# Optimization experiments

Hardware: AMD Instinct MI355X
Metric: run time of the kernel (lower is better)

The kernel has to match this reference:

```python
import jax, jax.numpy as jnp
import numpy as np

N = 100000        # total points across all graphs in the batch
NUM_THETAS = 64
BUMP_STEPS = 64
NUM_GRAPHS = 128  # data.batch.max() + 1
R = 1.0


def setup_inputs() -> dict:
    key = jax.random.key(0)
    k1, k2 = jax.random.split(key)
    x = jax.random.normal(k1, (N, 2), dtype=jnp.float32)
    # direction vectors on the circle, as in the module's Parameter init
    t = jnp.linspace(0.0, 2.0 * jnp.pi, NUM_THETAS)
    v = jnp.stack([jnp.sin(t), jnp.cos(t)], axis=1).astype(jnp.float32)  # [T, 2]
    lin = jnp.linspace(-R, R, BUMP_STEPS).astype(jnp.float32)            # [S]
    batch = jnp.sort(jax.random.randint(k2, (N,), 0, NUM_GRAPHS)).astype(jnp.int64)
    return {"x": x, "v": v, "lin": lin, "batch": batch}


def reference(x, v, lin, batch):
    # nh: projection of each point onto each direction -> [N, T]
    nh = x @ v.T
    # sigmoid bump over filtration heights: [S, N, T]
    ecc = jax.nn.sigmoid(200.0 * (lin[:, None, None] - nh[None, :, :]))
    # index_add over point dim keyed by graph id, then movedim(0,1):
    # transpose to [N, S, T] and segment-sum over N -> [B, S, T]
    out = jax.ops.segment_sum(jnp.transpose(ecc, (1, 0, 2)), batch,
                              num_segments=NUM_GRAPHS)
    return out
```

## Files before the change

### kernel.cpp

```cpp
#include <hip/hip_runtime.h>

#define NUM_GRAPHS 128
#define NUM_T 64
#define NUM_S 64
#define TPB 8
#define NTH (NUM_T/TPB)
#define NROWS 66

__global__ __launch_bounds__(512, 8) void ect_fused_kernel(
    const float2* __restrict__ x, const float* __restrict__ v,
    const int* __restrict__ batch, int n, float* __restrict__ out)
{
    constexpr float KD        = 9.1599685135807190f;
    constexpr float SCALE     = 1048576.0f;
    constexpr float INV_SCALE = 9.5367431640625e-07f;

    const int g   = blockIdx.x;
    const int th  = blockIdx.y;
    const int tid = (int)threadIdx.x;
    const int lane = tid & 63;
    const int tl   = lane & 7;
    const int pg   = lane >> 3;
    const int wv   = tid >> 6;

    __shared__ unsigned long long sm_w[NROWS * TPB];
    __shared__ unsigned sm_pref[NUM_S * TPB];
    __shared__ unsigned sm_seg[8 * TPB];
    __shared__ int sh_cnt[4];

    for (int i = tid; i < NROWS * TPB; i += 512) sm_w[i] = 0ull;
    if (tid < 4) sh_cnt[tid] = 0;
    __syncthreads();

    const int S = (n + 511) / 512;
    {
        const int pos = tid * S;
        const int val = (pos < n) ? batch[pos] : 0x7fffffff;
        const unsigned long long mA = __ballot(val < g);
        const unsigned long long mB = __ballot(val < g + 1);
        if ((tid & 63) == 0) {
            atomicAdd(&sh_cnt[0], (int)__popcll(mA));
            atomicAdd(&sh_cnt[1], (int)__popcll(mB));
        }
    }
    __syncthreads();
    const int cA = sh_cnt[0], cB = sh_cnt[1];
    const int baseA = (cA - 1) * S, baseB = (cB - 1) * S;
    {
        int a2 = 0, b2 = 0;
        for (int j = tid + 1; j <= S; j += 512) {
            if (cA >= 1) {
                const int p  = baseA + j;
                const int vv = (p < n) ? batch[p] : 0x7fffffff;
                a2 += (vv < g);
            }
            if (cB >= 1) {
                const int p  = baseB + j;
                const int vv = (p < n) ? batch[p] : 0x7fffffff;
                b2 += (vv < g + 1);
            }
        }
        const unsigned long long mA = __ballot(a2 != 0);
        const unsigned long long mB = __ballot(b2 != 0);
        if ((tid & 63) == 0) {
            atomicAdd(&sh_cnt[2], (int)__popcll(mA));
            atomicAdd(&sh_cnt[3], (int)__popcll(mB));
        }
    }
    __syncthreads();
    const int loA = (cA == 0) ? 0 : baseA + 1 + sh_cnt[2];
    const int loB = (cB == 0) ? 0 : baseB + 1 + sh_cnt[3];

    const int t = th * TPB + tl;
    const float w0t = 31.5f * v[2 * t];
    const float w1t = 31.5f * v[2 * t + 1];

    for (int ibase = loA + wv * 8; ibase < loB; ibase += 64) {
        const int j   = ibase + pg;
        const int jc  = min(j, loB - 1);
        const float2 p = x[jc];
        float w = fmaf(p.x, w0t, fmaf(p.y, w1t, 31.5f));
        if (j >= loB) w = 3.2e6f;
        float uc = rintf(w);
        uc = fminf(fmaxf(uc, -1.0f), 64.0f);
        const float d  = uc - w;
        const float E  = __builtin_amdgcn_exp2f(KD * d);
        const float r0 = __builtin_amdgcn_rcpf(1.0f + E);
        const unsigned u0 = (unsigned)fmaf(r0, -SCALE, SCALE + 0.5f);
        const int wr = (int)uc + 1;
        atomicAdd(&sm_w[(wr << 3) + tl],
                  (unsigned long long)u0 | (1ULL << 32));
    }
    __syncthreads();

    if (tid < 64) {
        const int seg = tid >> 3, col = tid & 7;
        unsigned run = 0;
        #pragma unroll
        for (int k = 0; k < 8; ++k) {
            const int wr = (seg << 3) + k;
            run += (unsigned)(sm_w[(wr << 3) + col] >> 32);
            sm_pref[(wr << 3) + col] = run;
        }
        sm_seg[(seg << 3) + col] = run;
    }
    __syncthreads();

    const int s   = tid >> 3;
    const int col = tid & 7;
    const int seg_i = s >> 3;
    unsigned off = 0;
    #pragma unroll
    for (int q = 0; q < 7; ++q)
        if (q < seg_i) off += sm_seg[(q << 3) + col];

    const unsigned bins = (unsigned)sm_w[((s + 1) << 3) + col];

    out[((size_t)g * NUM_S + s) * NUM_T + th * TPB + col] =
        (float)(off + sm_pref[(s << 3) + col]) + (float)bins * INV_SCALE;
}

extern "C" void kernel_launch(void* const* d_in, const int* in_sizes, int n_in,
                              void* d_out, int out_size, void* d_ws, size_t ws_size,
                              hipStream_t stream) {
    const float2* x   = (const float2*)d_in[0];
    const float*  v   = (const float*)d_in[1];
    const int*    bat = (const int*)d_in[3];
    float* out = (float*)d_out;
    const int n = in_sizes[3];

    ect_fused_kernel<<<dim3(NUM_GRAPHS, NTH), 512, 0, stream>>>(x, v, bat, n, out);
}
```

Measured before the change: 14.76 us.

## Replace exp/rcp sigmoid with odd polynomial and transpose shared bin layout

Swaps the exp2+rcp evaluation of the fractional sigmoid term for an odd degree-5 polynomial in the rounding residual, cutting transcendental instructions from the per-point inner loop. It also changes the shared-memory histogram from row-major [row][t] to [t][row], which alters bank mapping for the 64-bit atomics and the prefix/readout accesses. The polynomial is an approximation on |d|<=0.5, so the fractional contribution can differ from the true sigmoid, and near the clamped edge bins it no longer behaves like the original formula.

```diff
diff --git a/kernel.cpp b/kernel.cpp
--- a/kernel.cpp
+++ b/kernel.cpp
@@ -11,8 +11,11 @@
     const float2* __restrict__ x, const float* __restrict__ v,
     const int* __restrict__ batch, int n, float* __restrict__ out)
 {
-    constexpr float KD        = 9.1599685135807190f;
+    constexpr float C1 = 1.569095f;
+    constexpr float C3 = -4.224718f;
+    constexpr float C5 = 6.509020f;
     constexpr float SCALE     = 1048576.0f;
+    constexpr float HALFBIAS  = 524288.5f;
     constexpr float INV_SCALE = 9.5367431640625e-07f;
 
     const int g   = blockIdx.x;
@@ -23,12 +26,12 @@
     const int pg   = lane >> 3;
     const int wv   = tid >> 6;
 
-    __shared__ unsigned long long sm_w[NROWS * TPB];
+    __shared__ unsigned long long sm_w[TPB * NROWS];
     __shared__ unsigned sm_pref[NUM_S * TPB];
     __shared__ unsigned sm_seg[8 * TPB];
     __shared__ int sh_cnt[4];
 
-    for (int i = tid; i < NROWS * TPB; i += 512) sm_w[i] = 0ull;
+    for (int i = tid; i < TPB * NROWS; i += 512) sm_w[i] = 0ull;
     if (tid < 4) sh_cnt[tid] = 0;
     __syncthreads();
 
@@ -74,6 +77,7 @@
     const int t = th * TPB + tl;
     const float w0t = 31.5f * v[2 * t];
     const float w1t = 31.5f * v[2 * t + 1];
+    const int tlBase1 = tl * NROWS + 1;
 
     for (int ibase = loA + wv * 8; ibase < loB; ibase += 64) {
         const int j   = ibase + pg;
@@ -81,25 +85,26 @@
         const float2 p = x[jc];
         float w = fmaf(p.x, w0t, fmaf(p.y, w1t, 31.5f));
         if (j >= loB) w = 3.2e6f;
-        float uc = rintf(w);
-        uc = fminf(fmaxf(uc, -1.0f), 64.0f);
-        const float d  = uc - w;
-        const float E  = __builtin_amdgcn_exp2f(KD * d);
-        const float r0 = __builtin_amdgcn_rcpf(1.0f + E);
-        const unsigned u0 = (unsigned)fmaf(r0, -SCALE, SCALE + 0.5f);
-        const int wr = (int)uc + 1;
-        atomicAdd(&sm_w[(wr << 3) + tl],
+        const float ucf = rintf(w);
+        const float d   = ucf - w;
+        const float t2 = d * d;
+        const float pq = fmaf(fmaf(C5, t2, C3), t2, C1);
+        const float gv = pq * d;
+        const unsigned u0 = (unsigned)fmaf(gv, SCALE, HALFBIAS);
+        const int swi = max(min((int)ucf, 64), -1);
+        atomicAdd(&sm_w[tlBase1 + swi],
                   (unsigned long long)u0 | (1ULL << 32));
     }
     __syncthreads();
 
     if (tid < 64) {
         const int seg = tid >> 3, col = tid & 7;
+        const int cb  = col * NROWS;
         unsigned run = 0;
         #pragma unroll
         for (int k = 0; k < 8; ++k) {
             const int wr = (seg << 3) + k;
-            run += (unsigned)(sm_w[(wr << 3) + col] >> 32);
+            run += (unsigned)(sm_w[cb + wr] >> 32);
             sm_pref[(wr << 3) + col] = run;
         }
         sm_seg[(seg << 3) + col] = run;
@@ -114,7 +119,7 @@
     for (int q = 0; q < 7; ++q)
         if (q < seg_i) off += sm_seg[(q << 3) + col];
 
-    const unsigned bins = (unsigned)sm_w[((s + 1) << 3) + col];
+    const unsigned bins = (unsigned)sm_w[col * NROWS + (s + 1)];
 
     out[((size_t)g * NUM_S + s) * NUM_T + th * TPB + col] =
         (float)(off + sm_pref[(s << 3) + col]) + (float)bins * INV_SCALE;
```

Measured after the change: 13.87 us (median of 2 runs). 6.0% less time.
